# Performance work log

Measured on AMD Instinct MI355X. Metric: run time of the kernel, lower is better.

## Reference

```python
import jax, jax.numpy as jnp
import numpy as np

EMB = 1024
HEADS = 16
HEAD_DIM = EMB // HEADS
D_FF = 4 * EMB
EPS = 1e-5


def setup_inputs() -> dict:
    key = jax.random.key(0)
    ks = jax.random.split(key, 12)
    b, t = 4, 2048
    sc = 0.02
    return {
        "x": jax.random.normal(ks[0], (b, t, EMB), dtype=jnp.float32),
        # weights stored [in, out] (transpose of torch Linear.weight)
        "w_attn": jax.random.normal(ks[1], (EMB, 3 * EMB), dtype=jnp.float32) * sc,
        "b_attn": jnp.zeros((3 * EMB,), dtype=jnp.float32),
        "w_proj": jax.random.normal(ks[2], (EMB, EMB), dtype=jnp.float32) * sc,
        "b_proj": jnp.zeros((EMB,), dtype=jnp.float32),
        "ln1_g": jnp.ones((EMB,), dtype=jnp.float32),
        "ln1_b": jnp.zeros((EMB,), dtype=jnp.float32),
        "w_ff1": jax.random.normal(ks[3], (EMB, D_FF), dtype=jnp.float32) * sc,
        "b_ff1": jnp.zeros((D_FF,), dtype=jnp.float32),
        "w_ff2": jax.random.normal(ks[4], (D_FF, EMB), dtype=jnp.float32) * sc,
        "b_ff2": jnp.zeros((EMB,), dtype=jnp.float32),
        "ln2_g": jnp.ones((EMB,), dtype=jnp.float32),
        "ln2_b": jnp.zeros((EMB,), dtype=jnp.float32),
    }


def _layernorm(x, g, b):
    mu = jnp.mean(x, axis=-1, keepdims=True)
    var = jnp.var(x, axis=-1, keepdims=True)
    return (x - mu) * jax.lax.rsqrt(var + EPS) * g + b


def reference(x, w_attn, b_attn, w_proj, b_proj, ln1_g, ln1_b,
              w_ff1, b_ff1, w_ff2, b_ff2, ln2_g, ln2_b):
    b, t, e = x.shape
    h, s = HEADS, HEAD_DIM
    # fused qkv projection (GPT2-style c_attn)
    qkv = x @ w_attn + b_attn                      # [b, t, 3e]
    q, k, v = jnp.split(qkv, 3, axis=-1)
    q = q.reshape(b, t, h, s).transpose(0, 2, 1, 3)  # [b, h, t, s]
    k = k.reshape(b, t, h, s).transpose(0, 2, 1, 3)
    v = v.reshape(b, t, h, s).transpose(0, 2, 1, 3)
    dot = jnp.einsum('bhqs,bhks->bhqk', q, k) / jnp.sqrt(jnp.float32(s))
    # causal mask: mask_(..., mask_diagonal=False) zeroes i < j (strict upper)
    causal = jnp.tril(jnp.ones((t, t), dtype=bool))
    dot = jnp.where(causal, dot, jnp.float32(-jnp.inf))
    att = jax.nn.softmax(dot, axis=-1)
    out = jnp.einsum('bhqk,bhks->bhqs', att, v)    # [b, h, t, s]
    out = out.transpose(0, 2, 1, 3).reshape(b, t, e)
    attended = out @ w_proj + b_proj
    # residual + LayerNorm (dropout is identity in eval mode)
    x1 = _layernorm(attended + x, ln1_g, ln1_b)
    ff = jax.nn.relu(x1 @ w_ff1 + b_ff1) @ w_ff2 + b_ff2
    return _layernorm(ff + x1, ln2_g, ln2_b)
```

## Files before the change

kernel.cpp:

```cpp
#include <hip/hip_runtime.h>
#include <hip/hip_bf16.h>


typedef __attribute__((ext_vector_type(8))) short bf16x8;
typedef __attribute__((ext_vector_type(4))) float f32x4;

__device__ __forceinline__ unsigned short f2b(float f) {
  unsigned int u = __float_as_uint(f);
  u += 0x7fffu + ((u >> 16) & 1u);
  return (unsigned short)(u >> 16);
}
__device__ __forceinline__ unsigned int pk2b(float a, float b) {
  __hip_bfloat162 h = __float22bfloat162_rn(make_float2(a, b));
  return *(unsigned int*)&h;
}
__device__ __forceinline__ void gload_lds16(const unsigned short* g, unsigned short* l) {
  __builtin_amdgcn_global_load_lds((const __attribute__((address_space(1))) void*)g,
                                   (__attribute__((address_space(3))) void*)l, 16, 0, 0);
}

__global__ __launch_bounds__(256) void cvt_bf16(const float* __restrict__ in,
                                                unsigned short* __restrict__ out, long n) {
  long i = ((long)blockIdx.x * 256 + threadIdx.x) * 4;
  if (i >= n) return;
  float4 v = *(const float4*)(in + i);
  *(ushort4*)(out + i) = make_ushort4(f2b(v.x), f2b(v.y), f2b(v.z), f2b(v.w));
}

__global__ __launch_bounds__(256) void transpose_bf16(const float* __restrict__ in,
                                                      unsigned short* __restrict__ out,
                                                      int R, int C) {
  __shared__ float tile[32][33];
  int c0 = blockIdx.x * 32, r0 = blockIdx.y * 32;
  for (int i = threadIdx.y; i < 32; i += 8)
    tile[i][threadIdx.x] = in[(long)(r0 + i) * C + c0 + threadIdx.x];
  __syncthreads();
  for (int i = threadIdx.y; i < 32; i += 8)
    out[(long)(c0 + i) * R + r0 + threadIdx.x] = f2b(tile[threadIdx.x][i]);
}

template <int EPI>
__global__ __launch_bounds__(512, 2) void gemm256(const unsigned short* __restrict__ A,
                                                  const unsigned short* __restrict__ Bt,
                                                  const float* __restrict__ bias,
                                                  void* __restrict__ Cout,
                                                  void* __restrict__ Cout2,
                                                  int N, int K, int Kstride) {
  __shared__ __align__(16) unsigned short As[4][256 * 32];
  __shared__ __align__(16) unsigned short Bs[4][256 * 32];

  int tid = threadIdx.x;
  int wv = tid >> 6, lane = tid & 63, quad = lane >> 4, l16 = lane & 15;
  int wm = wv >> 2, wn = wv & 3;

  int nwg = gridDim.x, id = blockIdx.x;
  int sid = (id & 7) * (nwg >> 3) + (id >> 3);
  int bm256 = (sid & 31) * 256, bn256 = (sid >> 5) * 256;
  int chunk = blockIdx.y;
  long kbase = (long)chunk * K;

  int row1 = tid >> 2, row2 = row1 + 128;
  long dsl = ((tid & 3) ^ ((tid >> 3) & 3)) * 8;
  const unsigned short* Ap1 = A + (long)(bm256 + row1) * Kstride + kbase + dsl;
  const unsigned short* Ap2 = A + (long)(bm256 + row2) * Kstride + kbase + dsl;
  const unsigned short* Bp1 = Bt + (long)(bn256 + row1) * Kstride + kbase + dsl;
  const unsigned short* Bp2 = Bt + (long)(bn256 + row2) * Kstride + kbase + dsl;
  int lo1 = wv * 512, lo2 = wv * 512 + 4096;

  f32x4 acc[8][4] = {};
  int sl8 = (quad ^ ((l16 >> 1) & 3)) * 8;
  int arow = wm * 128 + l16;
  int brow = wn * 64 + l16;

  int NT = K >> 5;
  gload_lds16(Ap1, &As[0][lo1]); gload_lds16(Ap2, &As[0][lo2]);
  gload_lds16(Bp1, &Bs[0][lo1]); gload_lds16(Bp2, &Bs[0][lo2]);
  gload_lds16(Ap1 + 32, &As[1][lo1]); gload_lds16(Ap2 + 32, &As[1][lo2]);
  gload_lds16(Bp1 + 32, &Bs[1][lo1]); gload_lds16(Bp2 + 32, &Bs[1][lo2]);
  gload_lds16(Ap1 + 64, &As[2][lo1]); gload_lds16(Ap2 + 64, &As[2][lo2]);
  asm volatile("s_waitcnt vmcnt(6)\n\ts_barrier" ::: "memory");
  __builtin_amdgcn_sched_barrier(0);

  for (int tau = 0; tau < NT; ++tau) {
    const unsigned short* Ab = &As[tau & 3][0];
    const unsigned short* Bb = &Bs[tau & 3][0];
    bf16x8 af[4], bfr[4];
#pragma unroll
    for (int i = 0; i < 4; ++i)
      af[i] = *(const bf16x8*)(Ab + (arow + i * 16) * 32 + sl8);
#pragma unroll
    for (int j = 0; j < 4; ++j)
      bfr[j] = *(const bf16x8*)(Bb + (brow + j * 16) * 32 + sl8);
    if (tau + 2 < NT) {
      long ko = (long)(tau + 2) * 32;
      int s = (tau + 2) & 3;
      gload_lds16(Bp1 + ko, &Bs[s][lo1]);
      gload_lds16(Bp2 + ko, &Bs[s][lo2]);
    }
    asm volatile("s_barrier\n\ts_waitcnt lgkmcnt(0)" ::: "memory");
    __builtin_amdgcn_sched_barrier(0);
    __builtin_amdgcn_s_setprio(1);
#pragma unroll
    for (int i = 0; i < 4; ++i)
#pragma unroll
      for (int j = 0; j < 4; ++j)
        acc[i][j] = __builtin_amdgcn_mfma_f32_16x16x32_bf16(af[i], bfr[j], acc[i][j], 0, 0, 0);
    __builtin_amdgcn_s_setprio(0);
    __builtin_amdgcn_s_barrier();
    __builtin_amdgcn_sched_barrier(0);
    bf16x8 ag[4];
#pragma unroll
    for (int i = 0; i < 4; ++i)
      ag[i] = *(const bf16x8*)(Ab + (arow + (i + 4) * 16) * 32 + sl8);
    if (tau + 3 < NT) {
      long ko = (long)(tau + 3) * 32;
      int s = (tau + 3) & 3;
      gload_lds16(Ap1 + ko, &As[s][lo1]);
      gload_lds16(Ap2 + ko, &As[s][lo2]);
    }
    asm volatile("s_barrier\n\ts_waitcnt lgkmcnt(0)" ::: "memory");
    __builtin_amdgcn_sched_barrier(0);
    __builtin_amdgcn_s_setprio(1);
#pragma unroll
    for (int i = 0; i < 4; ++i)
#pragma unroll
      for (int j = 0; j < 4; ++j)
        acc[i + 4][j] = __builtin_amdgcn_mfma_f32_16x16x32_bf16(ag[i], bfr[j], acc[i + 4][j], 0, 0, 0);
    __builtin_amdgcn_s_setprio(0);
    if (tau + 3 < NT) {
      asm volatile("s_waitcnt vmcnt(6)\n\ts_barrier" ::: "memory");
    } else if (tau + 2 < NT) {
      asm volatile("s_waitcnt vmcnt(4)\n\ts_barrier" ::: "memory");
    } else if (tau + 1 < NT) {
      asm volatile("s_waitcnt vmcnt(0)\n\ts_barrier" ::: "memory");
    }
    __builtin_amdgcn_sched_barrier(0);
  }

  void* Cbase = chunk ? Cout2 : Cout;
#pragma unroll
  for (int i = 0; i < 8; ++i) {
#pragma unroll
    for (int j = 0; j < 4; ++j) {
      int gn = bn256 + wn * 64 + j * 16 + l16;
      float bv = chunk ? 0.f : bias[gn];
      if (EPI == 3 && gn >= 2048) {
        int h = (gn >> 6) & 15, s = gn & 63;
        int gm0 = bm256 + wm * 128 + i * 16 + quad * 4;
        int b = gm0 >> 11, tt0 = gm0 & 2047;
        unsigned short* vt = (unsigned short*)Cout + 16777216L;
        ushort4 us;
        us.x = f2b(acc[i][j][0] + bv);
        us.y = f2b(acc[i][j][1] + bv);
        us.z = f2b(acc[i][j][2] + bv);
        us.w = f2b(acc[i][j][3] + bv);
        *(ushort4*)(vt + (((long)(b * 16 + h)) * 64 + s) * 2048 + tt0) = us;
      } else {
#pragma unroll
        for (int r = 0; r < 4; ++r) {
          int gm = bm256 + wm * 128 + i * 16 + quad * 4 + r;
          float v = acc[i][j][r] + bv;
          if (EPI == 2) v = fmaxf(v, 0.f);
          if (EPI == 0) {
            ((float*)Cbase)[(long)gm * N + gn] = v;
          } else if (EPI == 2) {
            ((unsigned short*)Cbase)[(long)gm * N + gn] = f2b(v);
          } else {
            float sc = (gn < 1024) ? 0.18033688011112042f : 1.0f;
            ((unsigned short*)Cbase)[(long)gm * 2048 + gn] = f2b(v * sc);
          }
        }
      }
    }
  }
}

__global__ __launch_bounds__(256) void attn_mfma(const unsigned short* __restrict__ qkv,
                                                 unsigned short* __restrict__ outp) {
  const int LD = 72;
  __shared__ __align__(16) unsigned short Ks[64 * LD];
  __shared__ __align__(16) unsigned short Vts[64 * LD];
  __shared__ __align__(16) unsigned short Ps[4][16 * LD];
  int qa = blockIdx.x, qb = 31 - qa;
  int h = blockIdx.y, b = blockIdx.z;
  int t = threadIdx.x;
  int w = t >> 6, lane = t & 63, quad = lane >> 4, l16 = lane & 15;
  const unsigned short* qg = qkv + (long)(b * 2048) * 2048 + h * 64;
  const unsigned short* kg = qg + 1024;
  const unsigned short* vg = qkv + 16777216L + (((long)(b * 16 + h)) * 64) * 2048;
  unsigned short* Pw = &Ps[w][0];

  bf16x8 qfa[2], qfb[2];
#pragma unroll
  for (int ks = 0; ks < 2; ++ks) {
    qfa[ks] = *(const bf16x8*)(qg + (long)(qa * 64 + w * 16 + l16) * 2048 + ks * 32 + quad * 8);
    qfb[ks] = *(const bf16x8*)(qg + (long)(qb * 64 + w * 16 + l16) * 2048 + ks * 32 + quad * 8);
  }

  int sr = t >> 2, sc = (t & 3) * 16;
  const unsigned short* kp = kg + (long)sr * 2048 + sc;
  const unsigned short* vp = vg + (long)sr * 2048 + sc;
  int4 kv0 = *(const int4*)kp, kv1 = *(const int4*)(kp + 8);
  int4 vv0 = *(const int4*)vp, vv1 = *(const int4*)(vp + 8);
  kp += (long)64 * 2048;
  vp += 64;

  f32x4 oa[4] = {}, ob[4] = {};
  f32x4 la = {}, lb = {};
  const short ONE = 0x3F80;
  bf16x8 ones = {ONE, ONE, ONE, ONE, ONE, ONE, ONE, ONE};

  auto process = [&](const bf16x8* qf, int qt, int kt, f32x4* oacc, f32x4& lacc) {
    bool diag = (kt == qt);
#pragma unroll
    for (int rg = 0; rg < 4; ++rg) {
      bf16x8 kf0 = *(const bf16x8*)(Ks + (rg * 16 + l16) * LD + quad * 8);
      bf16x8 kf1 = *(const bf16x8*)(Ks + (rg * 16 + l16) * LD + 32 + quad * 8);
      f32x4 st = {};
      st = __builtin_amdgcn_mfma_f32_16x16x32_bf16(kf0, qf[0], st, 0, 0, 0);
      st = __builtin_amdgcn_mfma_f32_16x16x32_bf16(kf1, qf[1], st, 0, 0, 0);
      if (diag) {
        int kq = rg * 16 + quad * 4;
        int qq = w * 16 + l16;
#pragma unroll
        for (int r = 0; r < 4; ++r)
          if (kq + r > qq) st[r] = -1e30f;
      }
      unsigned int lo = pk2b(exp2f(st[0]), exp2f(st[1]));
      unsigned int hi = pk2b(exp2f(st[2]), exp2f(st[3]));
      *(uint2*)(Pw + l16 * LD + rg * 16 + quad * 4) = make_uint2(lo, hi);
    }
#pragma unroll
    for (int kc = 0; kc < 2; ++kc) {
      bf16x8 ap = *(const bf16x8*)(Pw + l16 * LD + kc * 32 + quad * 8);
      lacc = __builtin_amdgcn_mfma_f32_16x16x32_bf16(ap, ones, lacc, 0, 0, 0);
#pragma unroll
      for (int sg = 0; sg < 4; ++sg) {
        bf16x8 vf = *(const bf16x8*)(Vts + (sg * 16 + l16) * LD + kc * 32 + quad * 8);
        oacc[sg] = __builtin_amdgcn_mfma_f32_16x16x32_bf16(ap, vf, oacc[sg], 0, 0, 0);
      }
    }
  };

  for (int kt = 0; kt <= qb; ++kt) {
    __syncthreads();
    *(int4*)(Ks + sr * LD + sc) = kv0;
    *(int4*)(Ks + sr * LD + sc + 8) = kv1;
    *(int4*)(Vts + sr * LD + sc) = vv0;
    *(int4*)(Vts + sr * LD + sc + 8) = vv1;
    __syncthreads();
    if (kt < qb) {
      kv0 = *(const int4*)kp; kv1 = *(const int4*)(kp + 8);
      vv0 = *(const int4*)vp; vv1 = *(const int4*)(vp + 8);
      kp += (long)64 * 2048;
      vp += 64;
    }
    process(qfb, qb, kt, ob, lb);
    if (kt <= qa) process(qfa, qa, kt, oa, la);
  }

  auto epi = [&](int qt, f32x4* oacc, f32x4& lacc) {
#pragma unroll
    for (int r = 0; r < 4; ++r) {
      float invl = 1.f / lacc[r];
      int row = qt * 64 + w * 16 + quad * 4 + r;
      unsigned short* op = outp + ((long)(b * 2048 + row)) * 1024 + h * 64;
#pragma unroll
      for (int sg = 0; sg < 4; ++sg) op[sg * 16 + l16] = f2b(oacc[sg][r] * invl);
    }
  };
  epi(qa, oa, la);
  epi(qb, ob, lb);
}

__global__ __launch_bounds__(256) void ln_kernel(const float* __restrict__ a,
                                                 const float* __restrict__ a2,
                                                 const float* __restrict__ res,
                                                 const float* __restrict__ gam,
                                                 const float* __restrict__ bet,
                                                 float* __restrict__ outf,
                                                 unsigned short* __restrict__ outb) {
  int row = blockIdx.x, t = threadIdx.x;
  float4 av = *(const float4*)(a + (long)row * 1024 + t * 4);
  float4 rv = *(const float4*)(res + (long)row * 1024 + t * 4);
  float v0 = av.x + rv.x, v1 = av.y + rv.y, v2 = av.z + rv.z, v3 = av.w + rv.w;
  if (a2) {
    float4 a2v = *(const float4*)(a2 + (long)row * 1024 + t * 4);
    v0 += a2v.x; v1 += a2v.y; v2 += a2v.z; v3 += a2v.w;
  }
  float s = v0 + v1 + v2 + v3;
  float ss = v0 * v0 + v1 * v1 + v2 * v2 + v3 * v3;
#pragma unroll
  for (int off = 32; off >= 1; off >>= 1) {
    s += __shfl_down(s, off);
    ss += __shfl_down(ss, off);
  }
  __shared__ float sb[4], ssb[4];
  __shared__ float mean_s, inv_s;
  int w = t >> 6, lane = t & 63;
  if (lane == 0) { sb[w] = s; ssb[w] = ss; }
  __syncthreads();
  if (t == 0) {
    float S = sb[0] + sb[1] + sb[2] + sb[3];
    float SS = ssb[0] + ssb[1] + ssb[2] + ssb[3];
    float mean = S * (1.f / 1024.f);
    float var = SS * (1.f / 1024.f) - mean * mean;
    mean_s = mean;
    inv_s = rsqrtf(var + 1e-5f);
  }
  __syncthreads();
  float mean = mean_s, inv = inv_s;
  int c = t * 4;
  float4 gv = *(const float4*)(gam + c);
  float4 bv = *(const float4*)(bet + c);
  float y0 = (v0 - mean) * inv * gv.x + bv.x;
  float y1 = (v1 - mean) * inv * gv.y + bv.y;
  float y2 = (v2 - mean) * inv * gv.z + bv.z;
  float y3 = (v3 - mean) * inv * gv.w + bv.w;
  *(float4*)(outf + (long)row * 1024 + c) = make_float4(y0, y1, y2, y3);
  if (outb) {
    *(ushort4*)(outb + (long)row * 1024 + c) = make_ushort4(f2b(y0), f2b(y1), f2b(y2), f2b(y3));
  }
}

extern "C" void kernel_launch(void* const* d_in, const int* in_sizes, int n_in,
                              void* d_out, int out_size, void* d_ws, size_t ws_size,
                              hipStream_t stream) {
  const float* x      = (const float*)d_in[0];
  const float* w_attn = (const float*)d_in[1];
  const float* b_attn = (const float*)d_in[2];
  const float* w_proj = (const float*)d_in[3];
  const float* b_proj = (const float*)d_in[4];
  const float* ln1_g  = (const float*)d_in[5];
  const float* ln1_b  = (const float*)d_in[6];
  const float* w_ff1  = (const float*)d_in[7];
  const float* b_ff1  = (const float*)d_in[8];
  const float* w_ff2  = (const float*)d_in[9];
  const float* b_ff2  = (const float*)d_in[10];
  const float* ln2_g  = (const float*)d_in[11];
  const float* ln2_b  = (const float*)d_in[12];

  const long M = 8192, E = 1024;
  char* ws = (char*)d_ws;
  unsigned short* xb   = (unsigned short*)ws; ws += M * E * 2;
  unsigned short* wTa  = (unsigned short*)ws; ws += 3072L * 1024 * 2;
  unsigned short* wTp  = (unsigned short*)ws; ws += 1024L * 1024 * 2;
  unsigned short* wTf1 = (unsigned short*)ws; ws += 4096L * 1024 * 2;
  unsigned short* wTf2 = (unsigned short*)ws; ws += 4096L * 1024 * 2;
  unsigned short* qkvb = (unsigned short*)ws; ws += M * 3072 * 2;
  unsigned short* attb = (unsigned short*)ws; ws += M * E * 2;
  float* a1f = (float*)ws; ws += M * E * 4;
  float* x1f = (float*)ws; ws += M * E * 4;
  unsigned short* x1b = (unsigned short*)ws; ws += M * E * 2;
  unsigned short* hb = qkvb;
  float* f2 = a1f;
  float* prj1 = (float*)qkvb;
  float* ff21 = (float*)d_ws;

  cvt_bf16<<<dim3((M * E) / 4 / 256), dim3(256), 0, stream>>>(x, xb, M * E);
  transpose_bf16<<<dim3(3072 / 32, 1024 / 32), dim3(32, 8), 0, stream>>>(w_attn, wTa, 1024, 3072);
  transpose_bf16<<<dim3(1024 / 32, 1024 / 32), dim3(32, 8), 0, stream>>>(w_proj, wTp, 1024, 1024);
  transpose_bf16<<<dim3(4096 / 32, 1024 / 32), dim3(32, 8), 0, stream>>>(w_ff1, wTf1, 1024, 4096);
  transpose_bf16<<<dim3(1024 / 32, 4096 / 32), dim3(32, 8), 0, stream>>>(w_ff2, wTf2, 4096, 1024);
  gemm256<3><<<dim3(384, 1), dim3(512), 0, stream>>>(xb, wTa, b_attn, qkvb, nullptr, 3072, 1024, 1024);
  attn_mfma<<<dim3(16, 16, 4), dim3(256), 0, stream>>>(qkvb, attb);
  gemm256<0><<<dim3(128, 2), dim3(512), 0, stream>>>(attb, wTp, b_proj, a1f, prj1, 1024, 512, 1024);
  ln_kernel<<<dim3(8192), dim3(256), 0, stream>>>(a1f, prj1, x, ln1_g, ln1_b, x1f, x1b);
  gemm256<2><<<dim3(512, 1), dim3(512), 0, stream>>>(x1b, wTf1, b_ff1, hb, nullptr, 4096, 1024, 1024);
  gemm256<0><<<dim3(128, 2), dim3(512), 0, stream>>>(hb, wTf2, b_ff2, f2, ff21, 1024, 2048, 4096);
  ln_kernel<<<dim3(8192), dim3(256), 0, stream>>>(f2, ff21, x1f, ln2_g, ln2_b, (float*)d_out, nullptr);
}
```

Before: 567.1 us.

## Enlarge attention query tile to 128 rows and remap blocks for K/V locality

The attention kernel now processes 128-query tiles (two 16-row sub-tiles per wave) instead of 64, so each K/V tile loaded into shared memory feeds twice as many MFMAs. The grid becomes a flat 512-block launch with a swizzled mapping that groups blocks by (batch, head) so neighbouring blocks share K/V data in cache. The causal mask is generalised to the half-tile offset. This cuts K/V load and sync overhead per unit of compute, at the cost of more registers and a larger P buffer in shared memory, which may lower occupancy.

After: 585.6 us. 3.3% more time.

```diff
diff --git a/kernel.cpp b/kernel.cpp
--- a/kernel.cpp
+++ b/kernel.cpp
@@ -180,9 +180,11 @@
   const int LD = 72;
   __shared__ __align__(16) unsigned short Ks[64 * LD];
   __shared__ __align__(16) unsigned short Vts[64 * LD];
-  __shared__ __align__(16) unsigned short Ps[4][16 * LD];
-  int qa = blockIdx.x, qb = 31 - qa;
-  int h = blockIdx.y, b = blockIdx.z;
+  __shared__ __align__(16) unsigned short Ps[4][32 * LD];
+  int id = blockIdx.x;
+  int qa = (id >> 3) & 7, qb = 15 - qa;
+  int g = (id & 7) | ((id >> 6) << 3);
+  int h = g & 15, b = g >> 4;
   int t = threadIdx.x;
   int w = t >> 6, lane = t & 63, quad = lane >> 4, l16 = lane & 15;
   const unsigned short* qg = qkv + (long)(b * 2048) * 2048 + h * 64;
@@ -190,12 +192,14 @@
   const unsigned short* vg = qkv + 16777216L + (((long)(b * 16 + h)) * 64) * 2048;
   unsigned short* Pw = &Ps[w][0];
 
-  bf16x8 qfa[2], qfb[2];
-#pragma unroll
-  for (int ks = 0; ks < 2; ++ks) {
-    qfa[ks] = *(const bf16x8*)(qg + (long)(qa * 64 + w * 16 + l16) * 2048 + ks * 32 + quad * 8);
-    qfb[ks] = *(const bf16x8*)(qg + (long)(qb * 64 + w * 16 + l16) * 2048 + ks * 32 + quad * 8);
-  }
+  bf16x8 qfa[2][2], qfb[2][2];
+#pragma unroll
+  for (int qq = 0; qq < 2; ++qq)
+#pragma unroll
+    for (int ks = 0; ks < 2; ++ks) {
+      qfa[qq][ks] = *(const bf16x8*)(qg + (long)(qa * 128 + w * 32 + qq * 16 + l16) * 2048 + ks * 32 + quad * 8);
+      qfb[qq][ks] = *(const bf16x8*)(qg + (long)(qb * 128 + w * 32 + qq * 16 + l16) * 2048 + ks * 32 + quad * 8);
+    }
 
   int sr = t >> 2, sc = (t & 3) * 16;
   const unsigned short* kp = kg + (long)sr * 2048 + sc;
@@ -205,69 +209,81 @@
   kp += (long)64 * 2048;
   vp += 64;
 
-  f32x4 oa[4] = {}, ob[4] = {};
-  f32x4 la = {}, lb = {};
+  f32x4 oa[2][4] = {}, ob[2][4] = {};
+  f32x4 la[2] = {}, lb[2] = {};
   const short ONE = 0x3F80;
   bf16x8 ones = {ONE, ONE, ONE, ONE, ONE, ONE, ONE, ONE};
 
-  auto process = [&](const bf16x8* qf, int qt, int kt, f32x4* oacc, f32x4& lacc) {
-    bool diag = (kt == qt);
+  auto process = [&](const bf16x8 (&qf)[2][2], int qt2, int kt,
+                     f32x4 (&oacc)[2][4], f32x4 (&lacc)[2]) {
+    int rel = kt - qt2;
+    bool diag = (rel >= 0);
+    int off = rel << 6;
 #pragma unroll
     for (int rg = 0; rg < 4; ++rg) {
       bf16x8 kf0 = *(const bf16x8*)(Ks + (rg * 16 + l16) * LD + quad * 8);
       bf16x8 kf1 = *(const bf16x8*)(Ks + (rg * 16 + l16) * LD + 32 + quad * 8);
-      f32x4 st = {};
-      st = __builtin_amdgcn_mfma_f32_16x16x32_bf16(kf0, qf[0], st, 0, 0, 0);
-      st = __builtin_amdgcn_mfma_f32_16x16x32_bf16(kf1, qf[1], st, 0, 0, 0);
-      if (diag) {
-        int kq = rg * 16 + quad * 4;
-        int qq = w * 16 + l16;
-#pragma unroll
-        for (int r = 0; r < 4; ++r)
-          if (kq + r > qq) st[r] = -1e30f;
+#pragma unroll
+      for (int qq = 0; qq < 2; ++qq) {
+        f32x4 st = {};
+        st = __builtin_amdgcn_mfma_f32_16x16x32_bf16(kf0, qf[qq][0], st, 0, 0, 0);
+        st = __builtin_amdgcn_mfma_f32_16x16x32_bf16(kf1, qf[qq][1], st, 0, 0, 0);
+        if (diag) {
+          int kq = rg * 16 + quad * 4 + off;
+          int qrow = w * 32 + qq * 16 + l16;
+#pragma unroll
+          for (int r = 0; r < 4; ++r)
+            if (kq + r > qrow) st[r] = -1e30f;
+        }
+        unsigned int lo = pk2b(exp2f(st[0]), exp2f(st[1]));
+        unsigned int hi = pk2b(exp2f(st[2]), exp2f(st[3]));
+        *(uint2*)(Pw + (qq * 16 + l16) * LD + rg * 16 + quad * 4) = make_uint2(lo, hi);
       }
-      unsigned int lo = pk2b(exp2f(st[0]), exp2f(st[1]));
-      unsigned int hi = pk2b(exp2f(st[2]), exp2f(st[3]));
-      *(uint2*)(Pw + l16 * LD + rg * 16 + quad * 4) = make_uint2(lo, hi);
     }
 #pragma unroll
     for (int kc = 0; kc < 2; ++kc) {
-      bf16x8 ap = *(const bf16x8*)(Pw + l16 * LD + kc * 32 + quad * 8);
-      lacc = __builtin_amdgcn_mfma_f32_16x16x32_bf16(ap, ones, lacc, 0, 0, 0);
+      bf16x8 ap0 = *(const bf16x8*)(Pw + l16 * LD + kc * 32 + quad * 8);
+      bf16x8 ap1 = *(const bf16x8*)(Pw + (16 + l16) * LD + kc * 32 + quad * 8);
+      lacc[0] = __builtin_amdgcn_mfma_f32_16x16x32_bf16(ap0, ones, lacc[0], 0, 0, 0);
+      lacc[1] = __builtin_amdgcn_mfma_f32_16x16x32_bf16(ap1, ones, lacc[1], 0, 0, 0);
 #pragma unroll
       for (int sg = 0; sg < 4; ++sg) {
         bf16x8 vf = *(const bf16x8*)(Vts + (sg * 16 + l16) * LD + kc * 32 + quad * 8);
-        oacc[sg] = __builtin_amdgcn_mfma_f32_16x16x32_bf16(ap, vf, oacc[sg], 0, 0, 0);
+        oacc[0][sg] = __builtin_amdgcn_mfma_f32_16x16x32_bf16(ap0, vf, oacc[0][sg], 0, 0, 0);
+        oacc[1][sg] = __builtin_amdgcn_mfma_f32_16x16x32_bf16(ap1, vf, oacc[1][sg], 0, 0, 0);
       }
     }
   };
 
-  for (int kt = 0; kt <= qb; ++kt) {
+  int nkt = 2 * qb + 2;
+  for (int kt = 0; kt < nkt; ++kt) {
     __syncthreads();
     *(int4*)(Ks + sr * LD + sc) = kv0;
     *(int4*)(Ks + sr * LD + sc + 8) = kv1;
     *(int4*)(Vts + sr * LD + sc) = vv0;
     *(int4*)(Vts + sr * LD + sc + 8) = vv1;
     __syncthreads();
-    if (kt < qb) {
+    if (kt + 1 < nkt) {
       kv0 = *(const int4*)kp; kv1 = *(const int4*)(kp + 8);
       vv0 = *(const int4*)vp; vv1 = *(const int4*)(vp + 8);
       kp += (long)64 * 2048;
       vp += 64;
     }
-    process(qfb, qb, kt, ob, lb);
-    if (kt <= qa) process(qfa, qa, kt, oa, la);
-  }
-
-  auto epi = [&](int qt, f32x4* oacc, f32x4& lacc) {
-#pragma unroll
-    for (int r = 0; r < 4; ++r) {
-      float invl = 1.f / lacc[r];
-      int row = qt * 64 + w * 16 + quad * 4 + r;
-      unsigned short* op = outp + ((long)(b * 2048 + row)) * 1024 + h * 64;
-#pragma unroll
-      for (int sg = 0; sg < 4; ++sg) op[sg * 16 + l16] = f2b(oacc[sg][r] * invl);
-    }
+    process(qfb, 2 * qb, kt, ob, lb);
+    if (kt <= 2 * qa + 1) process(qfa, 2 * qa, kt, oa, la);
+  }
+
+  auto epi = [&](int qt, f32x4 (&oacc)[2][4], f32x4 (&lacc)[2]) {
+#pragma unroll
+    for (int qq = 0; qq < 2; ++qq)
+#pragma unroll
+      for (int r = 0; r < 4; ++r) {
+        float invl = 1.f / lacc[qq][r];
+        int row = qt * 128 + w * 32 + qq * 16 + quad * 4 + r;
+        unsigned short* op = outp + ((long)(b * 2048 + row)) * 1024 + h * 64;
+#pragma unroll
+        for (int sg = 0; sg < 4; ++sg) op[sg * 16 + l16] = f2b(oacc[qq][sg][r] * invl);
+      }
   };
   epi(qa, oa, la);
   epi(qb, ob, lb);
@@ -363,7 +379,7 @@
   transpose_bf16<<<dim3(4096 / 32, 1024 / 32), dim3(32, 8), 0, stream>>>(w_ff1, wTf1, 1024, 4096);
   transpose_bf16<<<dim3(1024 / 32, 4096 / 32), dim3(32, 8), 0, stream>>>(w_ff2, wTf2, 4096, 1024);
   gemm256<3><<<dim3(384, 1), dim3(512), 0, stream>>>(xb, wTa, b_attn, qkvb, nullptr, 3072, 1024, 1024);
-  attn_mfma<<<dim3(16, 16, 4), dim3(256), 0, stream>>>(qkvb, attb);
+  attn_mfma<<<dim3(512), dim3(256), 0, stream>>>(qkvb, attb);
   gemm256<0><<<dim3(128, 2), dim3(512), 0, stream>>>(attb, wTp, b_proj, a1f, prj1, 1024, 512, 1024);
   ln_kernel<<<dim3(8192), dim3(256), 0, stream>>>(a1f, prj1, x, ln1_g, ln1_b, x1f, x1b);
   gemm256<2><<<dim3(512, 1), dim3(512), 0, stream>>>(x1b, wTf1, b_ff1, hb, nullptr, 4096, 1024, 1024);
```
